# Optimization experiments

Measured on AMD Instinct MI355X. Metric: run time of the kernel, lower is better.

Reference implementation:

```python
import jax, jax.numpy as jnp
import numpy as np
import math

NUM_HEADS = 16
HEAD_SIZE = 64
QKT_MEAN = 0.0
QKT_STD = 0.05
APPLY_NOISE = True
NOISE_KEY = jax.random.key(42)


def quantize_activation_8bit(x):
    max_abs = jnp.maximum(jnp.max(jnp.abs(x)), 1e-08)
    scale = max_abs / 127.0
    return jnp.clip(jnp.round(x / scale), -127, 127) * scale


def quantize_weight_4bit(w):
    max_abs = jnp.maximum(jnp.max(jnp.abs(w)), 1e-08)
    scale = max_abs / 7.0
    return jnp.clip(jnp.round(w / scale), -7, 7) * scale


def setup_inputs() -> dict:
    key = jax.random.key(0)
    k1, k2, k3, k4 = jax.random.split(key, 4)
    B, S, D = 4, 1024, 1024
    hidden_states = jax.random.normal(k1, (B, S, D), dtype=jnp.float32)
    attention_mask = jnp.zeros((B, 1, 1, S), dtype=jnp.float32)
    # nn.Linear weights are [out_features, in_features]
    w_scale = 1.0 / math.sqrt(D)
    Wq = jax.random.normal(k2, (D, D), dtype=jnp.float32) * w_scale
    Wk = jax.random.normal(k3, (D, D), dtype=jnp.float32) * w_scale
    Wv = jax.random.normal(k4, (D, D), dtype=jnp.float32) * w_scale
    return {"hidden_states": hidden_states, "attention_mask": attention_mask,
            "Wq": Wq, "Wk": Wk, "Wv": Wv}


def _split_heads(x):
    B, S, _ = x.shape
    return x.reshape(B, S, NUM_HEADS, HEAD_SIZE).transpose(0, 2, 1, 3)  # [B,H,S,Dh]


def reference(hidden_states, attention_mask, Wq, Wk, Wv):
    h_q = quantize_activation_8bit(hidden_states)
    h_k = quantize_activation_8bit(hidden_states)
    Q = _split_heads(jnp.einsum('bsd,od->bso', h_q, quantize_weight_4bit(Wq)))
    K = _split_heads(jnp.einsum('bsd,od->bso', h_k, quantize_weight_4bit(Wk)))
    V = _split_heads(jnp.einsum('bsd,od->bso', hidden_states, quantize_weight_4bit(Wv)))
    qkt = jnp.einsum('bhqd,bhkd->bhqk', Q, K) / math.sqrt(HEAD_SIZE)
    if APPLY_NOISE and QKT_STD > 0:
        noise = jax.random.normal(NOISE_KEY, qkt.shape, dtype=qkt.dtype) * QKT_STD + QKT_MEAN
        qkt = qkt + noise
    qkt = qkt + attention_mask  # [B,1,1,S] broadcasts over [B,H,S,S]
    attn_weights = jax.nn.softmax(qkt, axis=-1)  # dropout is identity in eval
    ctx = jnp.einsum('bhqk,bhkd->bhqd', attn_weights, V)
    B, H, S, Dh = ctx.shape
    ctx = ctx.transpose(0, 2, 1, 3).reshape(B, S, H * Dh)
    return ctx
```

## Files before the change

kernel.cpp:

```cpp
#include <hip/hip_runtime.h>
#include <hip/hip_bf16.h>

typedef unsigned short u16;
typedef unsigned int u32;
typedef __bf16 bf16x8 __attribute__((ext_vector_type(8)));
typedef float f32x4 __attribute__((ext_vector_type(4)));

#define MFMA16(a, b, c) __builtin_amdgcn_mfma_f32_16x16x32_bf16((a), (b), (c), 0, 0, 0)

static __device__ __forceinline__ float bfbits2f(u32 b) {
    union { u32 u; float f; } c; c.u = b << 16; return c.f;
}
static __device__ __forceinline__ u32 f2bfbits(float f) {
    union { float f; u32 u; } c; c.f = f;
    return (c.u + 0x7FFFu + ((c.u >> 16) & 1u)) >> 16;
}
static __device__ __forceinline__ u32 f2bfbits_exact(float f) {
    union { float f; u32 u; } c; c.f = f;
    return c.u >> 16;
}

static __device__ __forceinline__ void threefry2x32(u32 c0, u32 c1, u32& o0, u32& o1) {
    const u32 k0 = 0u, k1 = 42u, k2 = 0u ^ 42u ^ 0x1BD11BDAu;
    u32 x0 = c0 + k0, x1 = c1 + k1;
#define TF_R4(ra, rb, rc, rd)                                   \
    x0 += x1; x1 = (x1 << ra) | (x1 >> (32 - ra)); x1 ^= x0;    \
    x0 += x1; x1 = (x1 << rb) | (x1 >> (32 - rb)); x1 ^= x0;    \
    x0 += x1; x1 = (x1 << rc) | (x1 >> (32 - rc)); x1 ^= x0;    \
    x0 += x1; x1 = (x1 << rd) | (x1 >> (32 - rd)); x1 ^= x0;
    TF_R4(13, 15, 26, 6)  x0 += k1; x1 += k2 + 1u;
    TF_R4(17, 29, 16, 24) x0 += k2; x1 += k0 + 2u;
    TF_R4(13, 15, 26, 6)  x0 += k0; x1 += k1 + 3u;
    TF_R4(17, 29, 16, 24) x0 += k1; x1 += k2 + 4u;
    TF_R4(13, 15, 26, 6)  x0 += k2; x1 += k0 + 5u;
#undef TF_R4
    o0 = x0; o1 = x1;
}

static __device__ __forceinline__ float noise_at(u32 idx) {
    u32 x0, x1;
    threefry2x32(0u, idx, x0, x1);
    u32 bits = x0 ^ x1;
    float f = __uint_as_float((bits >> 9) | 0x3F800000u) - 1.0f;
    float u = f * 2.0f - 0.99999994f;
    u = fmaxf(-0.99999994f, u);
    float t = fmaf(-u, u, 1.0f);
    float w = -__logf(t);
    float p;
    if (w < 5.0f) {
        float z = w - 2.5f;
        p = 2.81022636e-08f;
        p = fmaf(p, z, 3.43273939e-07f);
        p = fmaf(p, z, -3.5233877e-06f);
        p = fmaf(p, z, -4.39150654e-06f);
        p = fmaf(p, z, 0.00021858087f);
        p = fmaf(p, z, -0.00125372503f);
        p = fmaf(p, z, -0.00417768164f);
        p = fmaf(p, z, 0.246640727f);
        p = fmaf(p, z, 1.50140941f);
    } else {
        float z = sqrtf(w) - 3.0f;
        p = -0.000200214257f;
        p = fmaf(p, z, 0.000100950558f);
        p = fmaf(p, z, 0.00134934322f);
        p = fmaf(p, z, -0.00367342844f);
        p = fmaf(p, z, 0.00573950773f);
        p = fmaf(p, z, -0.0076224613f);
        p = fmaf(p, z, 0.00943887047f);
        p = fmaf(p, z, 1.00167406f);
        p = fmaf(p, z, 2.83297682f);
    }
    return (p * u) * 0.07071067811865475f;
}

__global__ __launch_bounds__(256) void absmax_k(const float* __restrict__ h,
                                                const float* __restrict__ wq,
                                                const float* __restrict__ wk,
                                                const float* __restrict__ wv,
                                                u32* __restrict__ slots) {
    int t = blockIdx.y;
    const float* src = (t == 0) ? h : (t == 1) ? wq : (t == 2) ? wk : wv;
    int n4 = ((t == 0) ? 4096 * 1024 : 1024 * 1024) / 4;
    u32 mx = 0;
    int tid = threadIdx.x;
    for (int i = blockIdx.x * blockDim.x + tid; i < n4; i += gridDim.x * blockDim.x) {
        uint4 v = ((const uint4*)src)[i];
        mx = max(mx, v.x & 0x7FFFFFFFu);
        mx = max(mx, v.y & 0x7FFFFFFFu);
        mx = max(mx, v.z & 0x7FFFFFFFu);
        mx = max(mx, v.w & 0x7FFFFFFFu);
    }
    __shared__ u32 red[256];
    red[tid] = mx;
    __syncthreads();
    for (int s = 128; s > 0; s >>= 1) {
        if (tid < s) red[tid] = max(red[tid], red[tid + s]);
        __syncthreads();
    }
    if (tid == 0) atomicMax(&slots[t], red[0]);
}

__global__ __launch_bounds__(256) void prequant(const float* __restrict__ src,
                                                u16* __restrict__ dqi,
                                                u16* __restrict__ draw,
                                                const u32* __restrict__ slots,
                                                int slot, float qmax, int n8) {
    float amax = fmaxf(__uint_as_float(slots[slot]), 1e-8f);
    float scale = amax / qmax;
    for (int i = blockIdx.x * blockDim.x + threadIdx.x; i < n8; i += gridDim.x * blockDim.x) {
        float4 a = ((const float4*)src)[2 * i];
        float4 b = ((const float4*)src)[2 * i + 1];
        float x[8] = {a.x, a.y, a.z, a.w, b.x, b.y, b.z, b.w};
        u16 qi[8], rw[8];
#pragma unroll
        for (int j = 0; j < 8; j++) {
            float q = fminf(fmaxf(rintf(x[j] / scale), -qmax), qmax);
            qi[j] = (u16)f2bfbits_exact(q);
            rw[j] = (u16)f2bfbits(x[j]);
        }
        *(uint4*)(dqi + 8 * (size_t)i) = *(const uint4*)qi;
        if (draw) *(uint4*)(draw + 8 * (size_t)i) = *(const uint4*)rw;
    }
}

__global__ __launch_bounds__(256) void qkv_gemm(const u16* __restrict__ A,
                                                const u16* __restrict__ Bw,
                                                const u32* __restrict__ slots,
                                                int wslot, int useAct, int transOut,
                                                u16* __restrict__ outp) {
    __shared__ __align__(16) u16 As[64 * 40];
    __shared__ __align__(16) u16 Bs[64 * 40];
    float s_a = fmaxf(__uint_as_float(slots[0]), 1e-8f) / 127.0f;
    float s_w = fmaxf(__uint_as_float(slots[wslot]), 1e-8f) / 7.0f;
    float oscale = useAct ? (s_a * s_w) : s_w;

    int tid = threadIdx.x;
    int srow = tid >> 2, scol = (tid & 3) * 8;
    int mbase = blockIdx.x * 64, nbase = blockIdx.y * 64;
    int lane = tid & 63, wv = tid >> 6;
    int quad = lane >> 4, l16 = lane & 15;

    f32x4 acc[4];
#pragma unroll
    for (int i = 0; i < 4; i++) acc[i] = (f32x4){0.f, 0.f, 0.f, 0.f};

    const u16* aptr = A + (size_t)(mbase + srow) * 1024 + scol;
    const u16* bptr = Bw + (size_t)(nbase + srow) * 1024 + scol;

    for (int k0 = 0; k0 < 1024; k0 += 32) {
        uint4 av = *(const uint4*)(aptr + k0);
        uint4 bv = *(const uint4*)(bptr + k0);
        __syncthreads();
        *(uint4*)(As + srow * 40 + scol) = av;
        *(uint4*)(Bs + srow * 40 + scol) = bv;
        __syncthreads();
        bf16x8 af = *(const bf16x8*)(As + (wv * 16 + l16) * 40 + quad * 8);
#pragma unroll
        for (int nt = 0; nt < 4; nt++) {
            bf16x8 bfr = *(const bf16x8*)(Bs + (nt * 16 + l16) * 40 + quad * 8);
            acc[nt] = MFMA16(af, bfr, acc[nt]);
        }
    }

#pragma unroll
    for (int nt = 0; nt < 4; nt++) {
#pragma unroll
        for (int r = 0; r < 4; r++) {
            float val = acc[nt][r] * oscale;
            int m = mbase + wv * 16 + quad * 4 + r;
            int o = nbase + nt * 16 + l16;
            int b = m >> 10, s = m & 1023;
            int hh = o >> 6, dh = o & 63;
            size_t off = transOut ? (((size_t)(b * 16 + hh) * 64 + dh) * 1024 + s)
                                  : (((size_t)(b * 16 + hh) * 1024 + s) * 64 + dh);
            outp[off] = (u16)f2bfbits(val);
        }
    }
}

__global__ __launch_bounds__(256) void attn_kernel(const u16* __restrict__ Q,
                                                   const u16* __restrict__ K,
                                                   const u16* __restrict__ Vt,
                                                   const float* __restrict__ mask,
                                                   float* __restrict__ outp) {
    __shared__ __align__(16) u16 Plds[2][4][16][40];
    int qt = blockIdx.x, h = blockIdx.y, b = blockIdx.z;
    int bh = b * 16 + h;
    int tid = threadIdx.x, wv = tid >> 6, lane = tid & 63;
    int quad = lane >> 4, l16 = lane & 15;
    int q0 = qt * 64 + wv * 16;

    const u16* Qb = Q + (size_t)bh * 1024 * 64;
    const u16* Kb = K + (size_t)bh * 1024 * 64;
    const u16* Vb = Vt + (size_t)bh * 64 * 1024;

    bf16x8 aq0 = *(const bf16x8*)(Qb + (q0 + l16) * 64 + quad * 8);
    bf16x8 aq1 = *(const bf16x8*)(Qb + (q0 + l16) * 64 + 32 + quad * 8);

    f32x4 oacc[4];
#pragma unroll
    for (int i = 0; i < 4; i++) oacc[i] = (f32x4){0.f, 0.f, 0.f, 0.f};
    float lsum[4] = {0.f, 0.f, 0.f, 0.f};

    u16* Pw0 = &Plds[0][wv][0][0];
    u16* Pw1 = &Plds[1][wv][0][0];
    u32 idxbase = ((u32)bh * 1024u + (u32)(q0 + quad * 4)) * 1024u;

    for (int ks = 0; ks < 1024; ks += 32) {
        f32x4 s0 = (f32x4){0.f, 0.f, 0.f, 0.f};
        f32x4 s1 = (f32x4){0.f, 0.f, 0.f, 0.f};
        const u16* Kt = Kb + (size_t)ks * 64;
        bf16x8 bk0 = *(const bf16x8*)(Kt + l16 * 64 + quad * 8);
        bf16x8 bk1 = *(const bf16x8*)(Kt + l16 * 64 + 32 + quad * 8);
        bf16x8 bk2 = *(const bf16x8*)(Kt + (16 + l16) * 64 + quad * 8);
        bf16x8 bk3 = *(const bf16x8*)(Kt + (16 + l16) * 64 + 32 + quad * 8);
        s0 = MFMA16(aq0, bk0, s0);
        s0 = MFMA16(aq1, bk1, s0);
        s1 = MFMA16(aq0, bk2, s1);
        s1 = MFMA16(aq1, bk3, s1);

        int kg0 = ks + l16;
        float mk0 = mask[b * 1024 + kg0];
        float mk1 = mask[b * 1024 + kg0 + 16];

        u16* myP = ((ks >> 5) & 1) ? Pw1 : Pw0;
#pragma unroll
        for (int r = 0; r < 4; r++) {
            u32 idx = idxbase + (u32)r * 1024u + (u32)kg0;
            float sv0 = s0[r] * 0.125f + noise_at(idx) + mk0;
            float sv1 = s1[r] * 0.125f + noise_at(idx + 16u) + mk1;
            u32 p0b = f2bfbits(__expf(sv0));
            u32 p1b = f2bfbits(__expf(sv1));
            myP[(quad * 4 + r) * 40 + l16] = (u16)p0b;
            myP[(quad * 4 + r) * 40 + 16 + l16] = (u16)p1b;
            lsum[r] += bfbits2f(p0b) + bfbits2f(p1b);
        }

        asm volatile("" ::: "memory");
        bf16x8 pf = *(const bf16x8*)(myP + l16 * 40 + quad * 8);
        asm volatile("" ::: "memory");
        const u16* Vk = Vb + ks;
#pragma unroll
        for (int nt = 0; nt < 4; nt++) {
            bf16x8 vf = *(const bf16x8*)(Vk + (nt * 16 + l16) * 1024 + quad * 8);
            oacc[nt] = MFMA16(pf, vf, oacc[nt]);
        }
    }

    float linv[4];
#pragma unroll
    for (int r = 0; r < 4; r++) {
        float l = lsum[r];
        l += __shfl_xor(l, 1);
        l += __shfl_xor(l, 2);
        l += __shfl_xor(l, 4);
        l += __shfl_xor(l, 8);
        linv[r] = 1.0f / l;
    }
#pragma unroll
    for (int nt = 0; nt < 4; nt++) {
#pragma unroll
        for (int r = 0; r < 4; r++) {
            int q = q0 + quad * 4 + r;
            int dh = nt * 16 + l16;
            outp[((size_t)(b * 1024 + q)) * 1024 + h * 64 + dh] = oacc[nt][r] * linv[r];
        }
    }
}

extern "C" void kernel_launch(void* const* d_in, const int* in_sizes, int n_in,
                              void* d_out, int out_size, void* d_ws, size_t ws_size,
                              hipStream_t stream) {
    (void)in_sizes; (void)n_in; (void)out_size; (void)ws_size;
    const float* hidden = (const float*)d_in[0];
    const float* maskp  = (const float*)d_in[1];
    const float* Wq     = (const float*)d_in[2];
    const float* Wk     = (const float*)d_in[3];
    const float* Wv     = (const float*)d_in[4];
    float* outp = (float*)d_out;

    char* ws = (char*)d_ws;
    u32* slots = (u32*)ws;
    u16* hq  = (u16*)(ws + 256);
    u16* hbf = hq + 4096 * 1024;
    u16* wqi = hbf + 4096 * 1024;
    u16* wki = wqi + 1024 * 1024;
    u16* wvi = wki + 1024 * 1024;
    u16* Qb  = wvi + 1024 * 1024;
    u16* Kb  = Qb + 4096 * 1024;
    u16* Vtb = Kb + 4096 * 1024;

    hipMemsetAsync(slots, 0, 16, stream);
    absmax_k<<<dim3(128, 4), 256, 0, stream>>>(hidden, Wq, Wk, Wv, slots);
    prequant<<<dim3(256), 256, 0, stream>>>(hidden, hq, hbf, slots, 0, 127.0f, 4096 * 1024 / 8);
    prequant<<<dim3(64), 256, 0, stream>>>(Wq, wqi, nullptr, slots, 1, 7.0f, 1024 * 1024 / 8);
    prequant<<<dim3(64), 256, 0, stream>>>(Wk, wki, nullptr, slots, 2, 7.0f, 1024 * 1024 / 8);
    prequant<<<dim3(64), 256, 0, stream>>>(Wv, wvi, nullptr, slots, 3, 7.0f, 1024 * 1024 / 8);
    qkv_gemm<<<dim3(64, 16), 256, 0, stream>>>(hq, wqi, slots, 1, 1, 0, Qb);
    qkv_gemm<<<dim3(64, 16), 256, 0, stream>>>(hq, wki, slots, 2, 1, 0, Kb);
    qkv_gemm<<<dim3(64, 16), 256, 0, stream>>>(hbf, wvi, slots, 3, 0, 1, Vtb);
    attn_kernel<<<dim3(16, 16, 4), 256, 0, stream>>>(Qb, Kb, Vtb, maskp, outp);
}
```

Before: 411.2 us.

## Batch prequant and QKV GEMM launches, streamline noise and bf16 packing

Merges the four prequant launches into one grid indexed by blockIdx.y, and the three QKV GEMM launches into one grid indexed by blockIdx.z. This removes launch gaps and lets the three GEMMs fill the device together. In the attention loop it uses a rotate builtin for threefry, drops the negation of the log, and folds the noise scale into fused multiply-adds. It also packs two probabilities with the hardware bf16x2 conversion. One risk: the hidden-state prequant now runs on 64 blocks instead of 256, which may leave that larger pass short of parallelism.

```diff
diff --git a/kernel.cpp b/kernel.cpp
--- a/kernel.cpp
+++ b/kernel.cpp
@@ -19,25 +19,27 @@
     union { float f; u32 u; } c; c.f = f;
     return c.u >> 16;
 }
+static __device__ __forceinline__ u32 pack_bf16x2(float lo, float hi) {
+    float2 v; v.x = lo; v.y = hi;
+    union { __hip_bfloat162 h; u32 u; } c;
+    c.h = __float22bfloat162_rn(v);
+    return c.u;
+}
 
 static __device__ __forceinline__ void threefry2x32(u32 c0, u32 c1, u32& o0, u32& o1) {
     const u32 k0 = 0u, k1 = 42u, k2 = 0u ^ 42u ^ 0x1BD11BDAu;
     u32 x0 = c0 + k0, x1 = c1 + k1;
-#define TF_R4(ra, rb, rc, rd)                                   \
-    x0 += x1; x1 = (x1 << ra) | (x1 >> (32 - ra)); x1 ^= x0;    \
-    x0 += x1; x1 = (x1 << rb) | (x1 >> (32 - rb)); x1 ^= x0;    \
-    x0 += x1; x1 = (x1 << rc) | (x1 >> (32 - rc)); x1 ^= x0;    \
-    x0 += x1; x1 = (x1 << rd) | (x1 >> (32 - rd)); x1 ^= x0;
-    TF_R4(13, 15, 26, 6)  x0 += k1; x1 += k2 + 1u;
-    TF_R4(17, 29, 16, 24) x0 += k2; x1 += k0 + 2u;
-    TF_R4(13, 15, 26, 6)  x0 += k0; x1 += k1 + 3u;
-    TF_R4(17, 29, 16, 24) x0 += k1; x1 += k2 + 4u;
-    TF_R4(13, 15, 26, 6)  x0 += k2; x1 += k0 + 5u;
-#undef TF_R4
+#define TF_R(r) x0 += x1; x1 = __builtin_rotateleft32(x1, r); x1 ^= x0;
+    TF_R(13) TF_R(15) TF_R(26) TF_R(6)   x0 += k1; x1 += k2 + 1u;
+    TF_R(17) TF_R(29) TF_R(16) TF_R(24)  x0 += k2; x1 += k0 + 2u;
+    TF_R(13) TF_R(15) TF_R(26) TF_R(6)   x0 += k0; x1 += k1 + 3u;
+    TF_R(17) TF_R(29) TF_R(16) TF_R(24)  x0 += k1; x1 += k2 + 4u;
+    TF_R(13) TF_R(15) TF_R(26) TF_R(6)   x0 += k2; x1 += k0 + 5u;
+#undef TF_R
     o0 = x0; o1 = x1;
 }
 
-static __device__ __forceinline__ float noise_at(u32 idx) {
+static __device__ __forceinline__ float noise_pu(u32 idx) {
     u32 x0, x1;
     threefry2x32(0u, idx, x0, x1);
     u32 bits = x0 ^ x1;
@@ -45,10 +47,10 @@
     float u = f * 2.0f - 0.99999994f;
     u = fmaxf(-0.99999994f, u);
     float t = fmaf(-u, u, 1.0f);
-    float w = -__logf(t);
+    float lg = __logf(t);
     float p;
-    if (w < 5.0f) {
-        float z = w - 2.5f;
+    if (lg > -5.0f) {
+        float z = fmaf(lg, -1.0f, -2.5f);
         p = 2.81022636e-08f;
         p = fmaf(p, z, 3.43273939e-07f);
         p = fmaf(p, z, -3.5233877e-06f);
@@ -59,7 +61,7 @@
         p = fmaf(p, z, 0.246640727f);
         p = fmaf(p, z, 1.50140941f);
     } else {
-        float z = sqrtf(w) - 3.0f;
+        float z = sqrtf(-lg) - 3.0f;
         p = -0.000200214257f;
         p = fmaf(p, z, 0.000100950558f);
         p = fmaf(p, z, 0.00134934322f);
@@ -70,7 +72,7 @@
         p = fmaf(p, z, 1.00167406f);
         p = fmaf(p, z, 2.83297682f);
     }
-    return (p * u) * 0.07071067811865475f;
+    return p * u;
 }
 
 __global__ __launch_bounds__(256) void absmax_k(const float* __restrict__ h,
@@ -100,12 +102,24 @@
     if (tid == 0) atomicMax(&slots[t], red[0]);
 }
 
-__global__ __launch_bounds__(256) void prequant(const float* __restrict__ src,
-                                                u16* __restrict__ dqi,
-                                                u16* __restrict__ draw,
-                                                const u32* __restrict__ slots,
-                                                int slot, float qmax, int n8) {
-    float amax = fmaxf(__uint_as_float(slots[slot]), 1e-8f);
+__global__ __launch_bounds__(256) void prequant_all(const float* __restrict__ hidden,
+                                                    const float* __restrict__ wq,
+                                                    const float* __restrict__ wk,
+                                                    const float* __restrict__ wv,
+                                                    u16* __restrict__ hq,
+                                                    u16* __restrict__ hbf,
+                                                    u16* __restrict__ wqi,
+                                                    u16* __restrict__ wki,
+                                                    u16* __restrict__ wvi,
+                                                    const u32* __restrict__ slots) {
+    int y = blockIdx.y;
+    const float* src = (y == 0) ? hidden : (y == 1) ? wq : (y == 2) ? wk : wv;
+    u16* dqi = (y == 0) ? hq : (y == 1) ? wqi : (y == 2) ? wki : wvi;
+    u16* draw = (y == 0) ? hbf : nullptr;
+    float qmax = (y == 0) ? 127.0f : 7.0f;
+    int n8 = ((y == 0) ? 4096 * 1024 : 1024 * 1024) / 8;
+
+    float amax = fmaxf(__uint_as_float(slots[y]), 1e-8f);
     float scale = amax / qmax;
     for (int i = blockIdx.x * blockDim.x + threadIdx.x; i < n8; i += gridDim.x * blockDim.x) {
         float4 a = ((const float4*)src)[2 * i];
@@ -123,16 +137,25 @@
     }
 }
 
-__global__ __launch_bounds__(256) void qkv_gemm(const u16* __restrict__ A,
-                                                const u16* __restrict__ Bw,
-                                                const u32* __restrict__ slots,
-                                                int wslot, int useAct, int transOut,
-                                                u16* __restrict__ outp) {
+__global__ __launch_bounds__(256) void qkv_gemm_all(const u16* __restrict__ hq,
+                                                    const u16* __restrict__ hbf,
+                                                    const u16* __restrict__ wqi,
+                                                    const u16* __restrict__ wki,
+                                                    const u16* __restrict__ wvi,
+                                                    const u32* __restrict__ slots,
+                                                    u16* __restrict__ Qb,
+                                                    u16* __restrict__ Kb,
+                                                    u16* __restrict__ Vtb) {
     __shared__ __align__(16) u16 As[64 * 40];
     __shared__ __align__(16) u16 Bs[64 * 40];
+    int z = blockIdx.z;
+    const u16* A  = (z < 2) ? hq : hbf;
+    const u16* Bw = (z == 0) ? wqi : (z == 1) ? wki : wvi;
+    u16* outp     = (z == 0) ? Qb : (z == 1) ? Kb : Vtb;
+    int transOut = (z == 2);
     float s_a = fmaxf(__uint_as_float(slots[0]), 1e-8f) / 127.0f;
-    float s_w = fmaxf(__uint_as_float(slots[wslot]), 1e-8f) / 7.0f;
-    float oscale = useAct ? (s_a * s_w) : s_w;
+    float s_w = fmaxf(__uint_as_float(slots[z + 1]), 1e-8f) / 7.0f;
+    float oscale = (z < 2) ? (s_a * s_w) : s_w;
 
     int tid = threadIdx.x;
     int srow = tid >> 2, scol = (tid & 3) * 8;
@@ -227,13 +250,14 @@
 #pragma unroll
         for (int r = 0; r < 4; r++) {
             u32 idx = idxbase + (u32)r * 1024u + (u32)kg0;
-            float sv0 = s0[r] * 0.125f + noise_at(idx) + mk0;
-            float sv1 = s1[r] * 0.125f + noise_at(idx + 16u) + mk1;
-            u32 p0b = f2bfbits(__expf(sv0));
-            u32 p1b = f2bfbits(__expf(sv1));
-            myP[(quad * 4 + r) * 40 + l16] = (u16)p0b;
-            myP[(quad * 4 + r) * 40 + 16 + l16] = (u16)p1b;
-            lsum[r] += bfbits2f(p0b) + bfbits2f(p1b);
+            float pu0 = noise_pu(idx);
+            float pu1 = noise_pu(idx + 16u);
+            float sv0 = fmaf(pu0, 0.07071067811865475f, fmaf(s0[r], 0.125f, mk0));
+            float sv1 = fmaf(pu1, 0.07071067811865475f, fmaf(s1[r], 0.125f, mk1));
+            u32 pk = pack_bf16x2(__expf(sv0), __expf(sv1));
+            myP[(quad * 4 + r) * 40 + l16] = (u16)pk;
+            myP[(quad * 4 + r) * 40 + 16 + l16] = (u16)(pk >> 16);
+            lsum[r] += bfbits2f(pk & 0xFFFFu) + bfbits2f(pk >> 16);
         }
 
         asm volatile("" ::: "memory");
@@ -292,12 +316,9 @@
 
     hipMemsetAsync(slots, 0, 16, stream);
     absmax_k<<<dim3(128, 4), 256, 0, stream>>>(hidden, Wq, Wk, Wv, slots);
-    prequant<<<dim3(256), 256, 0, stream>>>(hidden, hq, hbf, slots, 0, 127.0f, 4096 * 1024 / 8);
-    prequant<<<dim3(64), 256, 0, stream>>>(Wq, wqi, nullptr, slots, 1, 7.0f, 1024 * 1024 / 8);
-    prequant<<<dim3(64), 256, 0, stream>>>(Wk, wki, nullptr, slots, 2, 7.0f, 1024 * 1024 / 8);
-    prequant<<<dim3(64), 256, 0, stream>>>(Wv, wvi, nullptr, slots, 3, 7.0f, 1024 * 1024 / 8);
-    qkv_gemm<<<dim3(64, 16), 256, 0, stream>>>(hq, wqi, slots, 1, 1, 0, Qb);
-    qkv_gemm<<<dim3(64, 16), 256, 0, stream>>>(hq, wki, slots, 2, 1, 0, Kb);
-    qkv_gemm<<<dim3(64, 16), 256, 0, stream>>>(hbf, wvi, slots, 3, 0, 1, Vtb);
+    prequant_all<<<dim3(64, 4), 256, 0, stream>>>(hidden, Wq, Wk, Wv,
+                                                  hq, hbf, wqi, wki, wvi, slots);
+    qkv_gemm_all<<<dim3(64, 16, 3), 256, 0, stream>>>(hq, hbf, wqi, wki, wvi, slots,
+                                                      Qb, Kb, Vtb);
     attn_kernel<<<dim3(16, 16, 4), 256, 0, stream>>>(Qb, Kb, Vtb, maskp, outp);
 }
```

Result: faster. 392.2 us (-4.6%).
